# Performance work log

Hardware: AMD Instinct MI355X
Metric: run time of the kernel (lower is better)

## Reference

```python
import jax, jax.numpy as jnp
import numpy as np
import math

B, S, D, H, DK = 4, 2048, 512, 8, 64

def _xavier(key, shape):
    fan_in, fan_out = shape[-2], shape[-1]
    std = math.sqrt(2.0 / (fan_in + fan_out))
    return jax.random.normal(key, shape, dtype=jnp.float32) * std

def setup_inputs() -> dict:
    key = jax.random.key(0)
    ks = jax.random.split(key, 5)
    X = jax.random.normal(ks[0], (B, S, D), dtype=jnp.float32)
    W_q = _xavier(ks[1], (H, D, DK))
    W_k = _xavier(ks[2], (H, D, DK))
    W_v = _xavier(ks[3], (H, D, DK))
    W_o = _xavier(ks[4], (H * DK, D))
    return {"X": X, "W_q": W_q, "W_k": W_k, "W_v": W_v, "W_o": W_o}

def reference(X, W_q, W_k, W_v, W_o):
    d_k = W_q.shape[-1]
    # project all heads at once: [B,H,S,dk]
    Q = jnp.einsum('bsd,hdk->bhsk', X, W_q)
    K = jnp.einsum('bsd,hdk->bhsk', X, W_k)
    V = jnp.einsum('bsd,hdk->bhsk', X, W_v)
    scores = jnp.einsum('bhsk,bhtk->bhst', Q, K) / jnp.sqrt(jnp.asarray(d_k, X.dtype))
    seq_len = X.shape[1]
    causal = jnp.tril(jnp.ones((seq_len, seq_len), dtype=bool))  # strict upper -> -inf
    scores = jnp.where(causal[None, None, :, :], scores, -jnp.inf)
    attn = jax.nn.softmax(scores, axis=-1)
    out = jnp.einsum('bhst,bhtk->bhsk', attn, V)  # [B,H,S,dv]
    # original concat order: permute to (B,S,dv,H) then flatten -> head axis fastest
    Bx, Hx, Sx, DV = out.shape
    concat = jnp.transpose(out, (0, 2, 3, 1)).reshape(Bx, Sx, DV * Hx)
    return jnp.matmul(concat, W_o)
```

## Files before the change

kernel.cpp:

```cpp
#include <hip/hip_runtime.h>
#include <hip/hip_bf16.h>


typedef __bf16 bf16;
typedef __bf16 bf16x8 __attribute__((ext_vector_type(8)));
typedef __bf16 bf16x4 __attribute__((ext_vector_type(4)));
typedef __bf16 bf16x2 __attribute__((ext_vector_type(2)));
typedef float  f32x4  __attribute__((ext_vector_type(4)));
typedef float  f32x16 __attribute__((ext_vector_type(16)));
typedef unsigned int u32;
typedef u32 u32x4 __attribute__((ext_vector_type(4)));

#define AS1 __attribute__((address_space(1)))
#define AS3 __attribute__((address_space(3)))

__device__ __forceinline__ void async_lds16(const void* gsrc, void* ldst) {
  __builtin_amdgcn_global_load_lds((AS1 const void*)gsrc, (AS3 void*)ldst, 16, 0, 0);
}

__device__ __forceinline__ float fexp2(float x) {
  float r;
  asm("v_exp_f32 %0, %1" : "=v"(r) : "v"(x));
  return r;
}


__global__ __launch_bounds__(256) void k_cvt_x(const float4* __restrict__ X,
                                               bf16x4* __restrict__ Xb) {
  int i = blockIdx.x * 256 + threadIdx.x;
  float4 v = X[i];
  bf16x4 o = { (bf16)v.x, (bf16)v.y, (bf16)v.z, (bf16)v.w };
  Xb[i] = o;
}

__global__ __launch_bounds__(256) void k_build_w(const float* __restrict__ Wq,
                                                 const float* __restrict__ Wk,
                                                 const float* __restrict__ Wv,
                                                 const float* __restrict__ Wo,
                                                 bf16* __restrict__ BT,
                                                 bf16* __restrict__ WoT) {
  int idx = blockIdx.x * 256 + threadIdx.x;
  if (idx < 786432) {
    int n = idx >> 9, d = idx & 511;
    int which = n >> 9, h = (n >> 6) & 7, dk = n & 63;
    const float* W = (which == 0) ? Wq : ((which == 1) ? Wk : Wv);
    BT[idx] = (bf16)W[((h << 9) + d) * 64 + dk];
  } else {
    int i2 = idx - 786432;
    int d = i2 >> 9, c = i2 & 511;
    int h = c >> 6, dk = c & 63;
    WoT[i2] = (bf16)Wo[(((dk << 3) + h) << 9) + d];
  }
}


__device__ __forceinline__ void gemm_tile(const bf16* __restrict__ A,
                                          const bf16* __restrict__ BT,
                                          int K, int m0, int n0,
                                          char* sm, f32x4 acc[4][4]) {
  const int tid = threadIdx.x;
  const int lane = tid & 63, w = tid >> 6;
  const int wm = w >> 1, wn = w & 1;
  const int lr = lane & 15, lg = lane >> 4;
  for (int k0 = 0; k0 < K; k0 += 32) {
    __syncthreads();
    #pragma unroll
    for (int i = 0; i < 2; ++i) {
      int off16 = i * 256 + tid;
      int row   = off16 >> 2;
      int colb  = (off16 & 3) << 4;
      const char* srcA = (const char*)(A  + (m0 + row) * K + k0) + colb;
      const char* srcB = (const char*)(BT + (n0 + row) * K + k0) + colb;
      async_lds16(srcA, sm +        (i * 256 + w * 64) * 16);
      async_lds16(srcB, sm + 8192 + (i * 256 + w * 64) * 16);
    }
    __syncthreads();
    bf16x8 af[4], bfr[4];
    #pragma unroll
    for (int t = 0; t < 4; ++t) {
      af[t]  = *(const bf16x8*)(sm +        ((wm * 64 + t * 16 + lr) * 32 + 8 * lg) * 2);
      bfr[t] = *(const bf16x8*)(sm + 8192 + ((wn * 64 + t * 16 + lr) * 32 + 8 * lg) * 2);
    }
    #pragma unroll
    for (int am = 0; am < 4; ++am)
      #pragma unroll
      for (int bn = 0; bn < 4; ++bn)
        acc[am][bn] = __builtin_amdgcn_mfma_f32_16x16x32_bf16(af[am], bfr[bn], acc[am][bn], 0, 0, 0);
  }
}

__global__ __launch_bounds__(256) void k_gemm_qkv(const bf16* __restrict__ A,
                                                  const bf16* __restrict__ BT,
                                                  bf16* __restrict__ Qb,
                                                  bf16* __restrict__ Kb,
                                                  bf16* __restrict__ VTb) {
  __shared__ char sm[16384];
  const int m0 = blockIdx.y * 128, n0 = blockIdx.x * 128;
  f32x4 acc[4][4];
  #pragma unroll
  for (int a = 0; a < 4; ++a)
    #pragma unroll
    for (int b = 0; b < 4; ++b) { f32x4 z = {0.f,0.f,0.f,0.f}; acc[a][b] = z; }
  gemm_tile(A, BT, 512, m0, n0, sm, acc);
  const int lane = threadIdx.x & 63, w = threadIdx.x >> 6;
  const int wm = w >> 1, wn = w & 1, lr = lane & 15, lg = lane >> 4;
  const float qsc = 0.1803368801f;
  #pragma unroll
  for (int am = 0; am < 4; ++am)
    #pragma unroll
    for (int bn = 0; bn < 4; ++bn)
      #pragma unroll
      for (int r = 0; r < 4; ++r) {
        int m = m0 + wm * 64 + am * 16 + 4 * lg + r;
        int n = n0 + wn * 64 + bn * 16 + lr;
        int b = m >> 11, s = m & 2047;
        int which = n >> 9, h = (n >> 6) & 7, dk = n & 63;
        int bh = (b << 3) + h;
        float x = acc[am][bn][r];
        if (which == 0)      Qb[((bh << 11) + s) * 64 + dk] = (bf16)(x * qsc);
        else if (which == 1) Kb[((bh << 11) + s) * 64 + dk] = (bf16)x;
        else                 VTb[((bh << 6) + dk) * 2048 + s] = (bf16)x;
      }
}

__global__ __launch_bounds__(256) void k_gemm_out(const bf16* __restrict__ A,
                                                  const bf16* __restrict__ BT,
                                                  float* __restrict__ C) {
  __shared__ char sm[16384];
  const int m0 = blockIdx.y * 128, n0 = blockIdx.x * 128;
  f32x4 acc[4][4];
  #pragma unroll
  for (int a = 0; a < 4; ++a)
    #pragma unroll
    for (int b = 0; b < 4; ++b) { f32x4 z = {0.f,0.f,0.f,0.f}; acc[a][b] = z; }
  gemm_tile(A, BT, 512, m0, n0, sm, acc);
  const int lane = threadIdx.x & 63, w = threadIdx.x >> 6;
  const int wm = w >> 1, wn = w & 1, lr = lane & 15, lg = lane >> 4;
  #pragma unroll
  for (int am = 0; am < 4; ++am)
    #pragma unroll
    for (int bn = 0; bn < 4; ++bn)
      #pragma unroll
      for (int r = 0; r < 4; ++r) {
        int m = m0 + wm * 64 + am * 16 + 4 * lg + r;
        int n = n0 + wn * 64 + bn * 16 + lr;
        C[(m << 9) + n] = acc[am][bn][r];
      }
}


__device__ __forceinline__ void attn_stage(char* base, const bf16* Kh, const bf16* Vh,
                                           int tb, int tid) {
  #pragma unroll
  for (int k = 0; k < 2; ++k) {
    int s = tid + (k << 8);
    int row = s >> 3, g = s & 7;
    async_lds16((const void*)(Kh + ((tb + row) << 6) + ((g ^ (row & 7)) << 3)),
                base + s * 16);
  }
  #pragma unroll
  for (int k = 0; k < 2; ++k) {
    int s = tid + (k << 8);
    int row = s >> 3, g = s & 7;
    async_lds16((const void*)(Vh + (row << 11) + tb + ((g ^ (row & 7)) << 3)),
                base + 8192 + s * 16);
  }
}

__global__ __launch_bounds__(256, 2) void k_attn6(const bf16* __restrict__ Qb,
                                                  const bf16* __restrict__ Kb,
                                                  const bf16* __restrict__ VTb,
                                                  bf16* __restrict__ Oc) {
  __shared__ char sm[32768];
  const int tid = threadIdx.x, lane = tid & 63, wv = tid >> 6;
  const int l31 = lane & 31, hi = lane >> 5;
  const int bid = blockIdx.x;
  const int bh = bid & 31;
  const int qb = (bid < 256) ? (15 - (bid >> 5)) : ((bid - 256) >> 5);
  const int b = bh >> 3, h = bh & 7;
  const int q0 = qb << 7;
  const int wq0 = q0 + (wv << 5);
  const bf16* Qh = Qb  + ((size_t)bh << 17);
  const bf16* Kh = Kb  + ((size_t)bh << 17);
  const bf16* Vh = VTb + ((size_t)bh << 17);

  bf16x8 qf[4];
  #pragma unroll
  for (int kd = 0; kd < 4; ++kd)
    qf[kd] = *(const bf16x8*)(Qh + ((wq0 + l31) << 6) + kd * 16 + 8 * hi);

  f32x16 o0, o1;
  #pragma unroll
  for (int r = 0; r < 16; ++r) { o0[r] = 0.f; o1[r] = 0.f; }
  float m_run = -3e38f, lsum = 0.f;

  const int NT = (qb << 1) + 2;
  const int swz = l31 & 7;

  attn_stage(sm, Kh, Vh, 0, tid);

  for (int t = 0; t < NT; ++t) {
    const int tb = t << 6;
    char* cb = sm + ((t & 1) << 14);
    __syncthreads();
    if (t + 1 < NT)
      attn_stage(sm + (((t + 1) & 1) << 14), Kh, Vh, (t + 1) << 6, tid);
    if (tb > wq0 + 31) continue;

    f32x16 sA, sB;
    #pragma unroll
    for (int r = 0; r < 16; ++r) { sA[r] = 0.f; sB[r] = 0.f; }
    {
      bf16x8 kf[4];
      #pragma unroll
      for (int kd = 0; kd < 4; ++kd)
        kf[kd] = *(const bf16x8*)(cb + l31 * 128 + ((((kd << 1) + hi) ^ swz) << 4));
      __builtin_amdgcn_s_setprio(1);
      #pragma unroll
      for (int kd = 0; kd < 4; ++kd)
        sA = __builtin_amdgcn_mfma_f32_32x32x16_bf16(kf[kd], qf[kd], sA, 0, 0, 0);
      __builtin_amdgcn_s_setprio(0);
      #pragma unroll
      for (int kd = 0; kd < 4; ++kd)
        kf[kd] = *(const bf16x8*)(cb + (32 + l31) * 128 + ((((kd << 1) + hi) ^ swz) << 4));
      __builtin_amdgcn_s_setprio(1);
      #pragma unroll
      for (int kd = 0; kd < 4; ++kd)
        sB = __builtin_amdgcn_mfma_f32_32x32x16_bf16(kf[kd], qf[kd], sB, 0, 0, 0);
      __builtin_amdgcn_s_setprio(0);
    }

    const int sg = wq0 + l31;
    if (tb + 63 > wq0) {
      #pragma unroll
      for (int r = 0; r < 16; ++r) {
        int rk = tb + (r & 3) + 8 * (r >> 2) + 4 * hi;
        sA[r] = (rk > sg)      ? -1e30f : sA[r];
        sB[r] = (rk + 32 > sg) ? -1e30f : sB[r];
      }
    }
    float tv[16];
    #pragma unroll
    for (int r = 0; r < 16; ++r) tv[r] = fmaxf(sA[r], sB[r]);
    float m0_ = fmaxf(tv[0], tv[1]),  m1_ = fmaxf(tv[2], tv[3]);
    float m2_ = fmaxf(tv[4], tv[5]),  m3_ = fmaxf(tv[6], tv[7]);
    float m4_ = fmaxf(tv[8], tv[9]),  m5_ = fmaxf(tv[10], tv[11]);
    float m6_ = fmaxf(tv[12], tv[13]), m7_ = fmaxf(tv[14], tv[15]);
    float tmax = fmaxf(fmaxf(fmaxf(m0_, m1_), fmaxf(m2_, m3_)),
                       fmaxf(fmaxf(m4_, m5_), fmaxf(m6_, m7_)));
    float tms = fmaxf(tmax, __shfl_xor(tmax, 32));
    if (!__all(tms <= m_run + 8.f)) {
      float mn = fmaxf(m_run, tms);
      float fac = fexp2(m_run - mn);
      #pragma unroll
      for (int r = 0; r < 16; ++r) { o0[r] *= fac; o1[r] *= fac; }
      lsum *= fac;
      m_run = mn;
    }
    #pragma unroll
    for (int r = 0; r < 16; ++r) sA[r] = fexp2(sA[r] - m_run);
    #pragma unroll
    for (int r = 0; r < 16; ++r) sB[r] = fexp2(sB[r] - m_run);
    float a0 = (sA[0]+sB[0]) + (sA[1]+sB[1]),   a1 = (sA[2]+sB[2]) + (sA[3]+sB[3]);
    float a2 = (sA[4]+sB[4]) + (sA[5]+sB[5]),   a3 = (sA[6]+sB[6]) + (sA[7]+sB[7]);
    float a4 = (sA[8]+sB[8]) + (sA[9]+sB[9]),   a5 = (sA[10]+sB[10]) + (sA[11]+sB[11]);
    float a6 = (sA[12]+sB[12]) + (sA[13]+sB[13]), a7 = (sA[14]+sB[14]) + (sA[15]+sB[15]);
    float rs = ((a0 + a1) + (a2 + a3)) + ((a4 + a5) + (a6 + a7));
    lsum += rs + __shfl_xor(rs, 32);

    #pragma unroll
    for (int j = 0; j < 2; ++j) {
      u32 pk_[8];
      #pragma unroll
      for (int i = 0; i < 8; ++i) {
        float plo = j ? sB[2 * i] : sA[2 * i];
        float phi = j ? sB[2 * i + 1] : sA[2 * i + 1];
        bf16x2 pr = { (bf16)plo, (bf16)phi };
        pk_[i] = __builtin_bit_cast(u32, pr);
      }
      asm volatile("v_permlane32_swap_b32 %0, %1" : "+v"(pk_[0]), "+v"(pk_[2]));
      asm volatile("v_permlane32_swap_b32 %0, %1" : "+v"(pk_[1]), "+v"(pk_[3]));
      asm volatile("v_permlane32_swap_b32 %0, %1" : "+v"(pk_[4]), "+v"(pk_[6]));
      asm volatile("v_permlane32_swap_b32 %0, %1" : "+v"(pk_[5]), "+v"(pk_[7]));
      u32x4 w0 = { pk_[0], pk_[1], pk_[2], pk_[3] };
      u32x4 w1 = { pk_[4], pk_[5], pk_[6], pk_[7] };
      bf16x8 pb0 = __builtin_bit_cast(bf16x8, w0);
      bf16x8 pb1 = __builtin_bit_cast(bf16x8, w1);
      const char* vb = cb + 8192;
      bf16x8 v00 = *(const bf16x8*)(vb + l31 * 128        + ((((j << 2) + hi) ^ swz) << 4));
      bf16x8 v01 = *(const bf16x8*)(vb + l31 * 128        + ((((j << 2) + 2 + hi) ^ swz) << 4));
      bf16x8 v10 = *(const bf16x8*)(vb + (32 + l31) * 128 + ((((j << 2) + hi) ^ swz) << 4));
      bf16x8 v11 = *(const bf16x8*)(vb + (32 + l31) * 128 + ((((j << 2) + 2 + hi) ^ swz) << 4));
      __builtin_amdgcn_s_setprio(1);
      o0 = __builtin_amdgcn_mfma_f32_32x32x16_bf16(v00, pb0, o0, 0, 0, 0);
      o0 = __builtin_amdgcn_mfma_f32_32x32x16_bf16(v01, pb1, o0, 0, 0, 0);
      o1 = __builtin_amdgcn_mfma_f32_32x32x16_bf16(v10, pb0, o1, 0, 0, 0);
      o1 = __builtin_amdgcn_mfma_f32_32x32x16_bf16(v11, pb1, o1, 0, 0, 0);
      __builtin_amdgcn_s_setprio(0);
    }
  }

  float rn = 1.f / lsum;
  const int sg = wq0 + l31;
  bf16* Orow = Oc + (((size_t)((b << 11) + sg)) << 9) + (h << 6);
  #pragma unroll
  for (int g = 0; g < 4; ++g) {
    bf16x4 v0, v1;
    #pragma unroll
    for (int i = 0; i < 4; ++i) {
      v0[i] = (bf16)(o0[4 * g + i] * rn);
      v1[i] = (bf16)(o1[4 * g + i] * rn);
    }
    *(bf16x4*)(Orow + 4 * hi + 8 * g)      = v0;
    *(bf16x4*)(Orow + 32 + 4 * hi + 8 * g) = v1;
  }
}


extern "C" void kernel_launch(void* const* d_in, const int* in_sizes, int n_in,
                              void* d_out, int out_size, void* d_ws, size_t ws_size,
                              hipStream_t stream) {
  (void)in_sizes; (void)n_in; (void)out_size; (void)ws_size;
  const float* X  = (const float*)d_in[0];
  const float* Wq = (const float*)d_in[1];
  const float* Wk = (const float*)d_in[2];
  const float* Wv = (const float*)d_in[3];
  const float* Wo = (const float*)d_in[4];
  float* out = (float*)d_out;
  char* ws = (char*)d_ws;
  bf16* Xb   = (bf16*)(ws);
  bf16* Wqkv = (bf16*)(ws + 8388608);
  bf16* WoT  = (bf16*)(ws + 9961472);
  bf16* Qb   = (bf16*)(ws + 10485760);
  bf16* Kb   = (bf16*)(ws + 18874368);
  bf16* VTb  = (bf16*)(ws + 27262976);
  bf16* Oc   = (bf16*)(ws + 35651584);

  k_cvt_x<<<4096, 256, 0, stream>>>((const float4*)X, (bf16x4*)Xb);
  k_build_w<<<4096, 256, 0, stream>>>(Wq, Wk, Wv, Wo, Wqkv, WoT);
  k_gemm_qkv<<<dim3(12, 64), 256, 0, stream>>>(Xb, Wqkv, Qb, Kb, VTb);
  k_attn6<<<512, 256, 0, stream>>>(Qb, Kb, VTb, Oc);
  k_gemm_out<<<dim3(4, 64), 256, 0, stream>>>(Oc, WoT, out);
}
```

Baseline: 113.0 us.

## Double-buffer LDS in GEMM tile loop to overlap global loads with MFMA

Turns the projection GEMM main loop into a two-stage pipeline. It issues async global-to-LDS loads for the next K slice into a second buffer while MFMAs consume the current one, and needs only one barrier per iteration instead of two. It also raises wave priority around the MFMA block. Shared memory per block doubles to 32 KB, which may lower occupancy, and the GEMMs are only part of the total runtime, which is likely dominated by attention.

```diff
diff --git a/kernel.cpp b/kernel.cpp
--- a/kernel.cpp
+++ b/kernel.cpp
@@ -62,31 +62,46 @@
   const int lane = tid & 63, w = tid >> 6;
   const int wm = w >> 1, wn = w & 1;
   const int lr = lane & 15, lg = lane >> 4;
-  for (int k0 = 0; k0 < K; k0 += 32) {
-    __syncthreads();
-    #pragma unroll
-    for (int i = 0; i < 2; ++i) {
-      int off16 = i * 256 + tid;
-      int row   = off16 >> 2;
-      int colb  = (off16 & 3) << 4;
-      const char* srcA = (const char*)(A  + (m0 + row) * K + k0) + colb;
-      const char* srcB = (const char*)(BT + (n0 + row) * K + k0) + colb;
-      async_lds16(srcA, sm +        (i * 256 + w * 64) * 16);
-      async_lds16(srcB, sm + 8192 + (i * 256 + w * 64) * 16);
-    }
-    __syncthreads();
+#define GSTAGE(bi, k0) do {                                                        \
+    char* base_ = sm + ((bi) << 14);                                               \
+    _Pragma("unroll")                                                              \
+    for (int i_ = 0; i_ < 2; ++i_) {                                               \
+      int off_ = i_ * 256 + tid;                                                   \
+      int row_ = off_ >> 2, cb_ = (off_ & 3) << 4;                                 \
+      async_lds16((const char*)(A  + (m0 + row_) * K + (k0)) + cb_,                \
+                  base_ + off_ * 16);                                              \
+      async_lds16((const char*)(BT + (n0 + row_) * K + (k0)) + cb_,                \
+                  base_ + 8192 + off_ * 16);                                       \
+    }                                                                              \
+  } while (0)
+  const int NT = K >> 5;
+  GSTAGE(0, 0);
+  asm volatile("s_waitcnt vmcnt(0)" ::: "memory");
+  __builtin_amdgcn_s_barrier();
+  __builtin_amdgcn_sched_barrier(0);
+  for (int t = 0; t < NT; ++t) {
+    char* cb = sm + ((t & 1) << 14);
+    if (t + 1 < NT) GSTAGE((t + 1) & 1, (t + 1) << 5);
     bf16x8 af[4], bfr[4];
     #pragma unroll
-    for (int t = 0; t < 4; ++t) {
-      af[t]  = *(const bf16x8*)(sm +        ((wm * 64 + t * 16 + lr) * 32 + 8 * lg) * 2);
-      bfr[t] = *(const bf16x8*)(sm + 8192 + ((wn * 64 + t * 16 + lr) * 32 + 8 * lg) * 2);
-    }
+    for (int u = 0; u < 4; ++u) {
+      af[u]  = *(const bf16x8*)(cb +        ((wm * 64 + u * 16 + lr) * 32 + 8 * lg) * 2);
+      bfr[u] = *(const bf16x8*)(cb + 8192 + ((wn * 64 + u * 16 + lr) * 32 + 8 * lg) * 2);
+    }
+    __builtin_amdgcn_s_setprio(1);
     #pragma unroll
     for (int am = 0; am < 4; ++am)
       #pragma unroll
       for (int bn = 0; bn < 4; ++bn)
         acc[am][bn] = __builtin_amdgcn_mfma_f32_16x16x32_bf16(af[am], bfr[bn], acc[am][bn], 0, 0, 0);
-  }
+    __builtin_amdgcn_s_setprio(0);
+    if (t + 1 < NT) {
+      asm volatile("s_waitcnt vmcnt(0)" ::: "memory");
+      __builtin_amdgcn_s_barrier();
+      __builtin_amdgcn_sched_barrier(0);
+    }
+  }
+#undef GSTAGE
 }
 
 __global__ __launch_bounds__(256) void k_gemm_qkv(const bf16* __restrict__ A,
@@ -94,7 +109,7 @@
                                                   bf16* __restrict__ Qb,
                                                   bf16* __restrict__ Kb,
                                                   bf16* __restrict__ VTb) {
-  __shared__ char sm[16384];
+  __shared__ char sm[32768];
   const int m0 = blockIdx.y * 128, n0 = blockIdx.x * 128;
   f32x4 acc[4][4];
   #pragma unroll
@@ -126,7 +141,7 @@
 __global__ __launch_bounds__(256) void k_gemm_out(const bf16* __restrict__ A,
                                                   const bf16* __restrict__ BT,
                                                   float* __restrict__ C) {
-  __shared__ char sm[16384];
+  __shared__ char sm[32768];
   const int m0 = blockIdx.y * 128, n0 = blockIdx.x * 128;
   f32x4 acc[4][4];
   #pragma unroll
```

Result: faster. 92.47 us (-18.1%).
